# Kernel optimization log

Hardware: AMD Instinct MI355X
Metric: run time of the kernel (lower is better)

## Reference

```python
import jax, jax.numpy as jnp
import numpy as np

B, IN, H, G, WR = 8192, 1024, 1024, 2, 64
UR = [64, 64]


def setup_inputs() -> dict:
    key = jax.random.key(0)
    ks = jax.random.split(key, 9)
    hg = H // G
    return {
        "x": jax.random.normal(ks[0], (B, IN), jnp.float32),
        "h": jax.random.normal(ks[1], (B, H), jnp.float32),
        "c": jax.random.normal(ks[2], (B, H), jnp.float32),
        "u_x": 0.1 * jax.random.normal(ks[3], (IN, WR), jnp.float32),
        "v_x": 0.1 * jax.random.normal(ks[4], (4 * H, WR), jnp.float32),
        "u_h_0": 0.1 * jax.random.normal(ks[5], (G, hg, UR[0]), jnp.float32),
        "v_h_0": 0.1 * jax.random.normal(ks[6], (G, UR[0], 4 * hg), jnp.float32),
        "u_h_1": 0.1 * jax.random.normal(ks[7], (G, hg, UR[1]), jnp.float32),
        "v_h_1": 0.1 * jax.random.normal(ks[8], (G, UR[1], 4 * hg), jnp.float32),
        "bias_x": jnp.ones((1, 4 * H), jnp.float32),
        "bias_h": jnp.ones((1, 4 * H), jnp.float32),
    }


def reference(x, h, c, u_x, v_x, u_h_0, v_h_0, u_h_1, v_h_1, bias_x, bias_h):
    b = h.shape[0]
    hg = H // G
    # input-to-hidden low-rank projection: [B, 4H]
    gx = (x @ u_x) @ v_x.T + bias_x
    xf, xi, xn, xo = jnp.split(gx, 4, axis=1)  # each [B, H]

    hv = h.reshape(b, G, hg)  # [B, G, H/G]
    u_hs = [u_h_0, u_h_1]
    v_hs = [v_h_0, v_h_1]
    acc = None
    for i in range(G):
        # torch code rotates the group index list cumulatively each step:
        # step i uses permutation roll(arange(G), -i)
        perm = np.roll(np.arange(G), -i)
        h_op = hv[:, perm, :]  # [B, G, hg]
        t = jnp.einsum('bgd,gdr->bgr', h_op, u_hs[i])  # [B, G, r_i]
        t = jnp.einsum('bgr,grk->bgk', t, v_hs[i])     # [B, G, 4hg]
        acc = t if acc is None else acc + t

    # chunk along last dim into 4 gates, flatten group dim -> [B, H]
    f_h, i_h, n_h, o_h = [p.reshape(b, H) for p in jnp.split(acc, 4, axis=2)]
    hf, hi, hn, ho = jnp.split(bias_h, 4, axis=1)

    inputgate = jax.nn.sigmoid(xi + hi + i_h)
    forgetgate = jax.nn.sigmoid(xf + hf + f_h)
    outputgate = jax.nn.sigmoid(xo + ho + o_h)
    newgate = jnp.tanh(xn + hn + n_h)
    c_next = forgetgate * c + inputgate * newgate
    h_next = outputgate * jnp.tanh(c_next)
    return (h_next, c_next)
```

## Files before the change

kernel.cpp:

```cpp
#include <hip/hip_runtime.h>
#include <hip/hip_bf16.h>


typedef __bf16 bf16_t;
typedef __bf16 bf16x8 __attribute__((ext_vector_type(8)));
typedef float f32x4 __attribute__((ext_vector_type(4)));

#define MFMA16x16x32(a, b, c) __builtin_amdgcn_mfma_f32_16x16x32_bf16((a), (b), (c), 0, 0, 0)

#define T_OFF 0
#define UXT_OFF 5242880
#define UHT_OFF 5373952
#define WB_OFF 5636096

__global__ __launch_bounds__(256) void prep_kernel(
    const float* __restrict__ u_x, const float* __restrict__ u_h_0,
    const float* __restrict__ u_h_1, const float* __restrict__ v_h_0,
    const float* __restrict__ v_h_1, const float* __restrict__ v_x,
    bf16_t* __restrict__ uxT, bf16_t* __restrict__ uhT,
    bf16_t* __restrict__ Wb) {
  int i = blockIdx.x * 256 + threadIdx.x;
  if (i < 65536) {
    int j = i >> 10, k = i & 1023;
    uxT[i] = (bf16_t)u_x[k * 64 + j];
  } else if (i < 65536 + 131072) {
    int i2 = i - 65536;
    int s = i2 >> 15, rem = i2 & 32767;
    int j = rem >> 9, d = rem & 511;
    const float* src = (s & 1) ? u_h_1 : u_h_0;
    int goff = (s >> 1) ? 32768 : 0;
    uhT[i2] = (bf16_t)src[goff + d * 64 + j];
  } else if (i < 65536 + 131072 + 786432) {
    int e = i - 196608;
    int k = e % 192;
    int row = e / 192;
    int tile = row >> 7;
    int rr = row & 127;
    int g = tile >> 4, qt = tile & 15;
    int w = rr >> 5, ql = rr & 31;
    int m = g * 512 + qt * 32 + ql;
    int q = qt * 32 + ql;
    float val;
    if (k < 64)
      val = v_x[(w * 1024 + m) * 64 + k];
    else if (k < 128)
      val = v_h_0[g * 131072 + (k - 64) * 2048 + w * 512 + q];
    else
      val = v_h_1[g * 131072 + (k - 128) * 2048 + w * 512 + q];
    Wb[e] = (bf16_t)val;
  }
}

__global__ __launch_bounds__(256, 2) void phase1_kernel(
    const float* __restrict__ x, const float* __restrict__ h,
    const bf16_t* __restrict__ uxT, const bf16_t* __restrict__ uhT,
    bf16_t* __restrict__ T) {
  __shared__ bf16_t z[16][1048];
  const int b0 = blockIdx.x * 16;
  const int tid = threadIdx.x;
  const int wv = tid >> 6, lane = tid & 63;
  const int lo = lane & 15, quad = lane >> 4;
  const int srow = tid >> 4, sc = tid & 15;

  {
    const float* src = x + (size_t)(b0 + srow) * 1024;
#pragma unroll
    for (int j = 0; j < 16; ++j) {
      int col = sc * 4 + j * 64;
      float4 v = *(const float4*)(src + col);
      bf16_t* d = &z[srow][col];
      d[0] = (bf16_t)v.x; d[1] = (bf16_t)v.y;
      d[2] = (bf16_t)v.z; d[3] = (bf16_t)v.w;
    }
  }
  __syncthreads();

  f32x4 accx = {0.f, 0.f, 0.f, 0.f};
  {
    const bf16_t* wBase = uxT + (size_t)(16 * wv + lo) * 1024;
    for (int k = 0; k < 1024; k += 32) {
      bf16x8 af = *(const bf16x8*)&z[lo][k + quad * 8];
      bf16x8 bfr = *(const bf16x8*)(wBase + k + quad * 8);
      accx = MFMA16x16x32(af, bfr, accx);
    }
  }
#pragma unroll
  for (int r = 0; r < 4; ++r)
    T[(size_t)(b0 + quad * 4 + r) * 320 + 16 * wv + lo] = (bf16_t)accx[r];
  __syncthreads();

  {
    const float* src = h + (size_t)(b0 + srow) * 1024;
#pragma unroll
    for (int j = 0; j < 16; ++j) {
      int col = sc * 4 + j * 64;
      float4 v = *(const float4*)(src + col);
      bf16_t* d = &z[srow][col];
      d[0] = (bf16_t)v.x; d[1] = (bf16_t)v.y;
      d[2] = (bf16_t)v.z; d[3] = (bf16_t)v.w;
    }
  }
  __syncthreads();

  const int hoff = (wv == 1 || wv == 2) ? 512 : 0;
#pragma unroll
  for (int sub = 0; sub < 4; ++sub) {
    const bf16_t* wBase = uhT + (size_t)(wv * 64 + 16 * sub + lo) * 512;
    f32x4 acc = {0.f, 0.f, 0.f, 0.f};
    for (int k = 0; k < 512; k += 32) {
      bf16x8 af = *(const bf16x8*)&z[lo][hoff + k + quad * 8];
      bf16x8 bfr = *(const bf16x8*)(wBase + k + quad * 8);
      acc = MFMA16x16x32(af, bfr, acc);
    }
    int n = 64 + wv * 64 + sub * 16 + lo;
#pragma unroll
    for (int r = 0; r < 4; ++r)
      T[(size_t)(b0 + quad * 4 + r) * 320 + n] = (bf16_t)acc[r];
  }
}

__global__ __launch_bounds__(256, 3) void phase2_kernel(
    const bf16_t* __restrict__ T, const bf16_t* __restrict__ Wb,
    const float* __restrict__ bias_x, const float* __restrict__ bias_h,
    const float* __restrict__ c, float* __restrict__ out) {
  __shared__ bf16_t bs[128][200];

  const int b0 = blockIdx.x * 128;
  const int gq = blockIdx.y;
  const int g = gq >> 4, qt = gq & 15;
  const int tid = threadIdx.x;
  const int wv = tid >> 6, lane = tid & 63;
  const int lo = lane & 15, quad = lane >> 4;

  {
    const bf16_t* src = Wb + (size_t)gq * (128 * 192);
#pragma unroll
    for (int cch = 0; cch < 12; ++cch) {
      int lc = cch * 256 + tid;
      int row = lc / 24, col = (lc % 24) * 8;
      bf16x8 v = *(const bf16x8*)(src + (size_t)lc * 8);
      *(bf16x8*)&bs[row][col] = v;
    }
  }

  const int arow = b0 + wv * 32 + lo;
  bf16x8 a[2][6];
#pragma unroll
  for (int mt = 0; mt < 2; ++mt) {
    const bf16_t* tr = T + (size_t)(arow + mt * 16) * 320;
#pragma unroll
    for (int ks = 0; ks < 6; ++ks) {
      int col = (ks < 2) ? (ks * 32 + quad * 8)
                         : (64 + g * 128 + (ks - 2) * 32 + quad * 8);
      a[mt][ks] = *(const bf16x8*)(tr + col);
    }
  }
  __syncthreads();

  f32x4 acc[2][8];
#pragma unroll
  for (int mt = 0; mt < 2; ++mt)
#pragma unroll
    for (int nt = 0; nt < 8; ++nt) acc[mt][nt] = (f32x4){0.f, 0.f, 0.f, 0.f};

#pragma unroll
  for (int nt = 0; nt < 8; ++nt) {
#pragma unroll
    for (int ks = 0; ks < 6; ++ks) {
      bf16x8 bfr = *(const bf16x8*)&bs[nt * 16 + lo][ks * 32 + quad * 8];
      acc[0][nt] = MFMA16x16x32(a[0][ks], bfr, acc[0][nt]);
      acc[1][nt] = MFMA16x16x32(a[1][ks], bfr, acc[1][nt]);
    }
  }

  float bsum[4][2];
#pragma unroll
  for (int w = 0; w < 4; ++w)
#pragma unroll
    for (int cq = 0; cq < 2; ++cq) {
      int m = g * 512 + qt * 32 + cq * 16 + lo;
      int n = w * 1024 + m;
      bsum[w][cq] = bias_x[n] + bias_h[n];
    }

#pragma unroll
  for (int mt = 0; mt < 2; ++mt)
#pragma unroll
    for (int r = 0; r < 4; ++r) {
      int b = b0 + wv * 32 + mt * 16 + quad * 4 + r;
#pragma unroll
      for (int cq = 0; cq < 2; ++cq) {
        int m = g * 512 + qt * 32 + cq * 16 + lo;
        float fv = acc[mt][0 + cq][r] + bsum[0][cq];
        float iv = acc[mt][2 + cq][r] + bsum[1][cq];
        float nv = acc[mt][4 + cq][r] + bsum[2][cq];
        float ov = acc[mt][6 + cq][r] + bsum[3][cq];
        float cin = c[(size_t)b * 1024 + m];
        float ig = 1.f / (1.f + __expf(-iv));
        float fg = 1.f / (1.f + __expf(-fv));
        float og = 1.f / (1.f + __expf(-ov));
        float ng = tanhf(nv);
        float cn = fg * cin + ig * ng;
        float hn = og * tanhf(cn);
        out[(size_t)b * 1024 + m] = hn;
        out[8388608ull + (size_t)b * 1024 + m] = cn;
      }
    }
}

extern "C" void kernel_launch(void* const* d_in, const int* in_sizes, int n_in,
                              void* d_out, int out_size, void* d_ws,
                              size_t ws_size, hipStream_t stream) {
  const float* x = (const float*)d_in[0];
  const float* h = (const float*)d_in[1];
  const float* c = (const float*)d_in[2];
  const float* u_x = (const float*)d_in[3];
  const float* v_x = (const float*)d_in[4];
  const float* u_h_0 = (const float*)d_in[5];
  const float* v_h_0 = (const float*)d_in[6];
  const float* u_h_1 = (const float*)d_in[7];
  const float* v_h_1 = (const float*)d_in[8];
  const float* bias_x = (const float*)d_in[9];
  const float* bias_h = (const float*)d_in[10];

  char* ws = (char*)d_ws;
  bf16_t* T = (bf16_t*)(ws + T_OFF);
  bf16_t* uxT = (bf16_t*)(ws + UXT_OFF);
  bf16_t* uhT = (bf16_t*)(ws + UHT_OFF);
  bf16_t* Wb = (bf16_t*)(ws + WB_OFF);

  prep_kernel<<<3840, 256, 0, stream>>>(u_x, u_h_0, u_h_1, v_h_0, v_h_1, v_x,
                                        uxT, uhT, Wb);
  phase1_kernel<<<512, 256, 0, stream>>>(x, h, uxT, uhT, T);
  phase2_kernel<<<dim3(64, 32), 256, 0, stream>>>(T, Wb, bias_x, bias_h, c,
                                                  (float*)d_out);
}
```

Baseline: 233.1 us.

## Coalesce prep reads, interleave phase1 MFMAs, prefetch c/bias, use fast activations

The prep kernel now iterates over source elements so that fp32 weight reads are coalesced and the transposed bf16 writes are scattered, and it drops the per-element div/mod. Phase1 interleaves the four sub-tiles so each A fragment read from LDS feeds four MFMAs. Phase2 issues the c and bias loads before the GEMM so their latency overlaps compute. The activations switch to rcp-based sigmoid and exp-based tanh, which trades some accuracy for fewer instructions and adds overflow risk for large inputs.

```diff
diff --git a/kernel.cpp b/kernel.cpp
--- a/kernel.cpp
+++ b/kernel.cpp
@@ -12,6 +12,13 @@
 #define UXT_OFF 5242880
 #define UHT_OFF 5373952
 #define WB_OFF 5636096
+
+__device__ inline float fast_sigmoid(float x) {
+  return __builtin_amdgcn_rcpf(1.f + __expf(-x));
+}
+__device__ inline float fast_tanh(float x) {
+  return 2.f * __builtin_amdgcn_rcpf(1.f + __expf(-2.f * x)) - 1.f;
+}
 
 __global__ __launch_bounds__(256) void prep_kernel(
     const float* __restrict__ u_x, const float* __restrict__ u_h_0,
@@ -21,33 +28,36 @@
     bf16_t* __restrict__ Wb) {
   int i = blockIdx.x * 256 + threadIdx.x;
   if (i < 65536) {
-    int j = i >> 10, k = i & 1023;
-    uxT[i] = (bf16_t)u_x[k * 64 + j];
-  } else if (i < 65536 + 131072) {
+    int k = i >> 6, j = i & 63;
+    uxT[j * 1024 + k] = (bf16_t)u_x[i];
+  } else if (i < 196608) {
     int i2 = i - 65536;
-    int s = i2 >> 15, rem = i2 & 32767;
-    int j = rem >> 9, d = rem & 511;
-    const float* src = (s & 1) ? u_h_1 : u_h_0;
-    int goff = (s >> 1) ? 32768 : 0;
-    uhT[i2] = (bf16_t)src[goff + d * 64 + j];
-  } else if (i < 65536 + 131072 + 786432) {
-    int e = i - 196608;
-    int k = e % 192;
-    int row = e / 192;
-    int tile = row >> 7;
-    int rr = row & 127;
-    int g = tile >> 4, qt = tile & 15;
-    int w = rr >> 5, ql = rr & 31;
-    int m = g * 512 + qt * 32 + ql;
-    int q = qt * 32 + ql;
-    float val;
-    if (k < 64)
-      val = v_x[(w * 1024 + m) * 64 + k];
-    else if (k < 128)
-      val = v_h_0[g * 131072 + (k - 64) * 2048 + w * 512 + q];
-    else
-      val = v_h_1[g * 131072 + (k - 128) * 2048 + w * 512 + q];
-    Wb[e] = (bf16_t)val;
+    int uhs = i2 >> 16;
+    int rem = i2 & 65535;
+    int g = rem >> 15;
+    int d = (rem >> 6) & 511, j = rem & 63;
+    const float* src = uhs ? u_h_1 : u_h_0;
+    int s = g * 2 + uhs;
+    uhT[s * 32768 + j * 512 + d] = (bf16_t)src[rem];
+  } else if (i < 458752) {
+    int a = i - 196608;
+    int row = a >> 6, k = a & 63;
+    int w = row >> 10, m = row & 1023;
+    int g = m >> 9, q = m & 511;
+    int qt = q >> 5, ql = q & 31;
+    Wb[(g * 16 + qt) * 24576 + (w * 32 + ql) * 192 + k] = (bf16_t)v_x[a];
+  } else if (i < 720896) {
+    int b2 = i - 458752;
+    int g = b2 >> 17, r = (b2 >> 11) & 63, col = b2 & 2047;
+    int w = col >> 9, q = col & 511;
+    int qt = q >> 5, ql = q & 31;
+    Wb[(g * 16 + qt) * 24576 + (w * 32 + ql) * 192 + 64 + r] = (bf16_t)v_h_0[b2];
+  } else if (i < 983040) {
+    int c2 = i - 720896;
+    int g = c2 >> 17, r = (c2 >> 11) & 63, col = c2 & 2047;
+    int w = col >> 9, q = col & 511;
+    int qt = q >> 5, ql = q & 31;
+    Wb[(g * 16 + qt) * 24576 + (w * 32 + ql) * 192 + 128 + r] = (bf16_t)v_h_1[c2];
   }
 }
 
@@ -103,19 +113,26 @@
   __syncthreads();
 
   const int hoff = (wv == 1 || wv == 2) ? 512 : 0;
-#pragma unroll
-  for (int sub = 0; sub < 4; ++sub) {
-    const bf16_t* wBase = uhT + (size_t)(wv * 64 + 16 * sub + lo) * 512;
-    f32x4 acc = {0.f, 0.f, 0.f, 0.f};
+  f32x4 acc[4];
+#pragma unroll
+  for (int sub = 0; sub < 4; ++sub) acc[sub] = (f32x4){0.f, 0.f, 0.f, 0.f};
+  {
+    const bf16_t* wB = uhT + (size_t)(wv * 64 + lo) * 512;
     for (int k = 0; k < 512; k += 32) {
       bf16x8 af = *(const bf16x8*)&z[lo][hoff + k + quad * 8];
-      bf16x8 bfr = *(const bf16x8*)(wBase + k + quad * 8);
-      acc = MFMA16x16x32(af, bfr, acc);
-    }
+#pragma unroll
+      for (int sub = 0; sub < 4; ++sub) {
+        bf16x8 bfr = *(const bf16x8*)(wB + sub * (16 * 512) + k + quad * 8);
+        acc[sub] = MFMA16x16x32(af, bfr, acc[sub]);
+      }
+    }
+  }
+#pragma unroll
+  for (int sub = 0; sub < 4; ++sub) {
     int n = 64 + wv * 64 + sub * 16 + lo;
 #pragma unroll
     for (int r = 0; r < 4; ++r)
-      T[(size_t)(b0 + quad * 4 + r) * 320 + n] = (bf16_t)acc[r];
+      T[(size_t)(b0 + quad * 4 + r) * 320 + n] = (bf16_t)acc[sub][r];
   }
 }
 
@@ -155,6 +172,27 @@
       a[mt][ks] = *(const bf16x8*)(tr + col);
     }
   }
+
+  float cin[2][4][2];
+#pragma unroll
+  for (int mt = 0; mt < 2; ++mt)
+#pragma unroll
+    for (int r = 0; r < 4; ++r) {
+      int b = b0 + wv * 32 + mt * 16 + quad * 4 + r;
+#pragma unroll
+      for (int cq = 0; cq < 2; ++cq) {
+        int m = g * 512 + qt * 32 + cq * 16 + lo;
+        cin[mt][r][cq] = c[(size_t)b * 1024 + m];
+      }
+    }
+  float bsum[4][2];
+#pragma unroll
+  for (int w = 0; w < 4; ++w)
+#pragma unroll
+    for (int cq = 0; cq < 2; ++cq) {
+      int n = w * 1024 + g * 512 + qt * 32 + cq * 16 + lo;
+      bsum[w][cq] = bias_x[n] + bias_h[n];
+    }
   __syncthreads();
 
   f32x4 acc[2][8];
@@ -172,16 +210,6 @@
       acc[1][nt] = MFMA16x16x32(a[1][ks], bfr, acc[1][nt]);
     }
   }
-
-  float bsum[4][2];
-#pragma unroll
-  for (int w = 0; w < 4; ++w)
-#pragma unroll
-    for (int cq = 0; cq < 2; ++cq) {
-      int m = g * 512 + qt * 32 + cq * 16 + lo;
-      int n = w * 1024 + m;
-      bsum[w][cq] = bias_x[n] + bias_h[n];
-    }
 
 #pragma unroll
   for (int mt = 0; mt < 2; ++mt)
@@ -195,13 +223,12 @@
         float iv = acc[mt][2 + cq][r] + bsum[1][cq];
         float nv = acc[mt][4 + cq][r] + bsum[2][cq];
         float ov = acc[mt][6 + cq][r] + bsum[3][cq];
-        float cin = c[(size_t)b * 1024 + m];
-        float ig = 1.f / (1.f + __expf(-iv));
-        float fg = 1.f / (1.f + __expf(-fv));
-        float og = 1.f / (1.f + __expf(-ov));
-        float ng = tanhf(nv);
-        float cn = fg * cin + ig * ng;
-        float hn = og * tanhf(cn);
+        float ig = fast_sigmoid(iv);
+        float fg = fast_sigmoid(fv);
+        float og = fast_sigmoid(ov);
+        float ng = fast_tanh(nv);
+        float cn = fg * cin[mt][r][cq] + ig * ng;
+        float hn = og * fast_tanh(cn);
         out[(size_t)b * 1024 + m] = hn;
         out[8388608ull + (size_t)b * 1024 + m] = cn;
       }
```

Result: faster. 210.0 us (-9.9%).
